# Kernel tuning notes

Measured on AMD Instinct MI355X. Metric: run time of the kernel, lower is better.

The kernel has to match this reference:

```python
import jax, jax.numpy as jnp
import numpy as np

DMIN, DMAX = -1.0, 1.0
B, I, O, K = 1024, 256, 256, 128

def setup_inputs() -> dict:
    key = jax.random.key(0)
    k1, k2, k3 = jax.random.split(key, 3)
    x = jax.random.normal(k1, (B, I), dtype=jnp.float32)
    bound = 1.0 / np.sqrt(I)
    base_weight = jax.random.uniform(k2, (O, I), dtype=jnp.float32, minval=-bound, maxval=bound)
    coeff = 0.03 * jax.random.normal(k3, (O, I, K), dtype=jnp.float32)
    coeff = coeff - coeff.mean(axis=-1, keepdims=True)
    return {
        'x': x,
        'base_weight': base_weight,
        'spline_coefficients': coeff,
        'spline_scale': jnp.ones((O, I), dtype=jnp.float32),
        'bias': jnp.zeros((O,), dtype=jnp.float32),
    }


def reference(x, base_weight, spline_coefficients, spline_scale, bias):
    num_knots = spline_coefficients.shape[-1]
    step = (DMAX - DMIN) / (num_knots - 1)
    # input activation (tanh) then clamp to spline domain
    p = jnp.tanh(x)                                   # (B, I)
    c = jnp.clip(p, DMIN, DMAX)
    scaled = (c - DMIN) / step                        # in [0, K-1]
    left = jnp.clip(jnp.floor(scaled).astype(jnp.int32), 0, num_knots - 1)
    right = jnp.minimum(left + 1, num_knots - 1)
    frac = scaled - left.astype(p.dtype)              # (B, I)
    # fold spline_scale into coefficients, then gather only the 2 relevant knots
    Cs = spline_coefficients * spline_scale[..., None]  # (O, I, K)
    ii = jnp.arange(x.shape[1])[None, :]                # (1, I) broadcasts with (B, I)
    cl = Cs[:, ii, left]                                # (O, B, I)
    cr = Cs[:, ii, right]                               # (O, B, I)
    spline = jnp.einsum('bi,obi->bo', 1.0 - frac, cl) + jnp.einsum('bi,obi->bo', frac, cr)
    base = jax.nn.silu(p) @ base_weight.T               # (B, O)
    return base + spline + bias[None, :]
```

## Files before the change

kernel.cpp:

```cpp
#include <hip/hip_runtime.h>

constexpr int Bb = 1024;
constexpr int Ii = 256;
constexpr int Oo = 256;
constexpr int Kk = 128;
constexpr int NCH = 8;

typedef unsigned short u16;
typedef unsigned int u32;
typedef u16 ushort4v __attribute__((ext_vector_type(4)));

__device__ __forceinline__ float bf16u_to_f(u16 u) {
    union { u32 ui; float f; } c;
    c.ui = ((u32)u) << 16;
    return c.f;
}
__device__ __forceinline__ u16 f_to_bf16(float f) {
    union { float f; u32 u; } c; c.f = f;
    u32 r = c.u + 0x7fffu + ((c.u >> 16) & 1u);
    return (u16)(r >> 16);
}

__global__ __launch_bounds__(256) void kperm(const float* __restrict__ cs,
                                             const float* __restrict__ scale,
                                             const float* __restrict__ wbase,
                                             u16* __restrict__ cp,
                                             float* __restrict__ wt) {
    __shared__ u16 T[128 * 66];
    int blk = blockIdx.x;
    int chunk = blk & 7;
    int sub = blk >> 3;
    int i  = chunk * 32 + (sub & 31);
    int oh = (sub >> 5) & 1, kh = (sub >> 6) & 1;
    int o0 = oh << 7, kb = kh << 6;
    int t = threadIdx.x;

    {
        int c4 = t & 15;
        int rb = t >> 4;
        const float4* cs4 = (const float4*)cs;
#pragma unroll
        for (int p = 0; p < 8; ++p) {
            int r = p * 16 + rb;
            int o = o0 + r;
            float sc = scale[o * Ii + i];
            float4 val = cs4[(size_t)(o * Ii + i) * (Kk / 4) + kh * 16 + c4];
            int kl = c4 * 4;
            T[r * 66 + kl + 0] = f_to_bf16(val.x * sc);
            T[r * 66 + kl + 1] = f_to_bf16(val.y * sc);
            T[r * 66 + kl + 2] = f_to_bf16(val.z * sc);
            T[r * 66 + kl + 3] = f_to_bf16(val.w * sc);
        }
    }
    __syncthreads();
    {
        int og = t & 63;
        int kg = t >> 6;
#pragma unroll
        for (int m = 0; m < 16; ++m) {
            int kl = kg * 16 + m;
            u32 lo = T[(og * 2) * 66 + kl];
            u32 hi = T[(og * 2 + 1) * 66 + kl];
            *(u32*)&cp[((size_t)i * Kk + kb + kl) * Oo + o0 + og * 2] = lo | (hi << 16);
        }
    }
    if (blk < 256) {
        int gid = blk * 256 + t;
        wt[gid] = wbase[(gid & 255) * Ii + (gid >> 8)];
    }
}

__global__ __launch_bounds__(256, 4) void kmain(const float* __restrict__ x,
                                                const char* __restrict__ cpb,
                                                const float* __restrict__ wt,
                                                float4* __restrict__ part4) {
    __shared__ float4 sf[256];
    __shared__ float wbuf[8 * 256];
    int t = threadIdx.x;
    int blk = blockIdx.x;
    int chunk = blk & (NCH - 1);
    int b0 = (blk >> 3) << 3;
    int i0 = chunk << 5;

    {
        int il = t & 31, bl = t >> 5;
        float xv = x[(size_t)(b0 + bl) * Ii + i0 + il];
        float e2 = __expf(2.f * xv);
        float p = 1.f - 2.f / (e2 + 1.f);
        float s = p / (1.f + __expf(-p));
        float c = fminf(fmaxf(p, -1.f), 1.f);
        float scaled = (c + 1.f) * ((float)(Kk - 1) * 0.5f);
        int l = (int)floorf(scaled);
        l = min(max(l, 0), Kk - 1);
        int rr = min(l + 1, Kk - 1);
        float4 v;
        v.x = scaled - (float)l;
        v.y = s;
        v.z = __int_as_float(l * (Oo * 2));
        v.w = __int_as_float(rr * (Oo * 2));
        sf[il * 8 + bl] = v;
    }

    int oq = t & 63;
    int bq = t >> 6;

    float a00=0.f,a01=0.f,a02=0.f,a03=0.f;
    float a10=0.f,a11=0.f,a12=0.f,a13=0.f;
    const char* cbase = cpb + (size_t)i0 * (Kk * Oo * 2) + oq * 8;

#pragma unroll
    for (int jb = 0; jb < 4; ++jb) {
        __syncthreads();
        {
            const float* wsrc = wt + (size_t)(i0 + jb * 8) * Oo;
#pragma unroll
            for (int p = 0; p < 8; ++p)
                wbuf[t + p * 256] = wsrc[t + p * 256];
        }
        __syncthreads();
#pragma unroll 4
        for (int m = 0; m < 8; ++m) {
            int il = jb * 8 + m;
            float4 v0 = sf[il * 8 + bq * 2];
            float4 v1 = sf[il * 8 + bq * 2 + 1];
            float4 w = *(const float4*)&wbuf[m * 256 + oq * 4];
            const char* ci = cbase + (size_t)il * (Kk * Oo * 2);
            ushort4v cl0 = *(const ushort4v*)(ci + __float_as_int(v0.z));
            ushort4v cr0 = *(const ushort4v*)(ci + __float_as_int(v0.w));
            ushort4v cl1 = *(const ushort4v*)(ci + __float_as_int(v1.z));
            ushort4v cr1 = *(const ushort4v*)(ci + __float_as_int(v1.w));
            float f0 = v0.x, g0 = 1.f - v0.x, s0 = v0.y;
            float f1 = v1.x, g1 = 1.f - v1.x, s1 = v1.y;
            a00 = fmaf(s0, w.x, a00); a01 = fmaf(s0, w.y, a01);
            a02 = fmaf(s0, w.z, a02); a03 = fmaf(s0, w.w, a03);
            a10 = fmaf(s1, w.x, a10); a11 = fmaf(s1, w.y, a11);
            a12 = fmaf(s1, w.z, a12); a13 = fmaf(s1, w.w, a13);
            a00 = fmaf(g0, bf16u_to_f(cl0.x), a00); a00 = fmaf(f0, bf16u_to_f(cr0.x), a00);
            a01 = fmaf(g0, bf16u_to_f(cl0.y), a01); a01 = fmaf(f0, bf16u_to_f(cr0.y), a01);
            a02 = fmaf(g0, bf16u_to_f(cl0.z), a02); a02 = fmaf(f0, bf16u_to_f(cr0.z), a02);
            a03 = fmaf(g0, bf16u_to_f(cl0.w), a03); a03 = fmaf(f0, bf16u_to_f(cr0.w), a03);
            a10 = fmaf(g1, bf16u_to_f(cl1.x), a10); a10 = fmaf(f1, bf16u_to_f(cr1.x), a10);
            a11 = fmaf(g1, bf16u_to_f(cl1.y), a11); a11 = fmaf(f1, bf16u_to_f(cr1.y), a11);
            a12 = fmaf(g1, bf16u_to_f(cl1.z), a12); a12 = fmaf(f1, bf16u_to_f(cr1.z), a12);
            a13 = fmaf(g1, bf16u_to_f(cl1.w), a13); a13 = fmaf(f1, bf16u_to_f(cr1.w), a13);
        }
    }
    size_t cstride = (size_t)(Bb * Oo / 4);
    float4 r0; r0.x=a00; r0.y=a01; r0.z=a02; r0.w=a03;
    float4 r1; r1.x=a10; r1.y=a11; r1.z=a12; r1.w=a13;
    part4[chunk * cstride + (size_t)(b0 + bq * 2) * (Oo / 4) + oq] = r0;
    part4[chunk * cstride + (size_t)(b0 + bq * 2 + 1) * (Oo / 4) + oq] = r1;
}

__global__ __launch_bounds__(256) void kreduce(const float4* __restrict__ part4,
                                               const float4* __restrict__ bias4,
                                               float4* __restrict__ out4) {
    int gid = blockIdx.x * 256 + threadIdx.x;
    const float4* p = part4 + gid;
    float4 s = p[0];
#pragma unroll
    for (int c = 1; c < NCH; ++c) {
        float4 v = p[(size_t)c * (Bb * Oo / 4)];
        s.x += v.x; s.y += v.y; s.z += v.z; s.w += v.w;
    }
    float4 bv = bias4[gid & 63];
    s.x += bv.x; s.y += bv.y; s.z += bv.z; s.w += bv.w;
    out4[gid] = s;
}

extern "C" void kernel_launch(void* const* d_in, const int* in_sizes, int n_in,
                              void* d_out, int out_size, void* d_ws, size_t ws_size,
                              hipStream_t stream) {
    const float* x     = (const float*)d_in[0];
    const float* wbase = (const float*)d_in[1];
    const float* coeff = (const float*)d_in[2];
    const float* scale = (const float*)d_in[3];
    const float* bias  = (const float*)d_in[4];
    float* out = (float*)d_out;

    char* ws = (char*)d_ws;
    u16*    cp    = (u16*)ws;
    float*  wt    = (float*)(ws + (16u << 20));
    float4* part4 = (float4*)(ws + (17u << 20));

    kperm<<<1024, 256, 0, stream>>>(coeff, scale, wbase, cp, wt);
    kmain<<<1024, 256, 0, stream>>>(x, (const char*)cp, wt, part4);
    kreduce<<<(Bb * Oo / 4) / 256, 256, 0, stream>>>(part4, (const float4*)bias, (float4*)out);
}
```

Baseline: 109.2 us.

## Fuse split-I reduction into main kernel via last-arrival atomic counter

Removes the separate reduce kernel launch. Each kmain block increments a per-batch-tile atomic counter after writing its partials, and the last of the eight chunk blocks for a tile sums the partials, adds the bias and writes the output. The counters are zeroed in kperm. This saves one kernel launch and its pass over global memory, at the cost of a threadfence, an atomic per block, and a serialized tail on the last-arriving block.

```diff
diff --git a/kernel.cpp b/kernel.cpp
--- a/kernel.cpp
+++ b/kernel.cpp
@@ -25,7 +25,8 @@
                                              const float* __restrict__ scale,
                                              const float* __restrict__ wbase,
                                              u16* __restrict__ cp,
-                                             float* __restrict__ wt) {
+                                             float* __restrict__ wt,
+                                             u32* __restrict__ cnt) {
     __shared__ u16 T[128 * 66];
     int blk = blockIdx.x;
     int chunk = blk & 7;
@@ -68,18 +69,24 @@
         int gid = blk * 256 + t;
         wt[gid] = wbase[(gid & 255) * Ii + (gid >> 8)];
     }
+    if (blk == 256 && t < 128) cnt[t] = 0;
 }
 
 __global__ __launch_bounds__(256, 4) void kmain(const float* __restrict__ x,
                                                 const char* __restrict__ cpb,
                                                 const float* __restrict__ wt,
-                                                float4* __restrict__ part4) {
+                                                float4* __restrict__ part4,
+                                                u32* __restrict__ cnt,
+                                                const float4* __restrict__ bias4,
+                                                float4* __restrict__ out4) {
     __shared__ float4 sf[256];
     __shared__ float wbuf[8 * 256];
+    __shared__ int lastArrival;
     int t = threadIdx.x;
     int blk = blockIdx.x;
     int chunk = blk & (NCH - 1);
-    int b0 = (blk >> 3) << 3;
+    int bt = blk >> 3;
+    int b0 = bt << 3;
     int i0 = chunk << 5;
 
     {
@@ -150,22 +157,33 @@
     float4 r1; r1.x=a10; r1.y=a11; r1.z=a12; r1.w=a13;
     part4[chunk * cstride + (size_t)(b0 + bq * 2) * (Oo / 4) + oq] = r0;
     part4[chunk * cstride + (size_t)(b0 + bq * 2 + 1) * (Oo / 4) + oq] = r1;
-}
-
-__global__ __launch_bounds__(256) void kreduce(const float4* __restrict__ part4,
-                                               const float4* __restrict__ bias4,
-                                               float4* __restrict__ out4) {
-    int gid = blockIdx.x * 256 + threadIdx.x;
-    const float4* p = part4 + gid;
-    float4 s = p[0];
-#pragma unroll
-    for (int c = 1; c < NCH; ++c) {
-        float4 v = p[(size_t)c * (Bb * Oo / 4)];
-        s.x += v.x; s.y += v.y; s.z += v.z; s.w += v.w;
-    }
-    float4 bv = bias4[gid & 63];
-    s.x += bv.x; s.y += bv.y; s.z += bv.z; s.w += bv.w;
-    out4[gid] = s;
+
+    __threadfence();
+    __syncthreads();
+    if (t == 0) {
+        u32 old = __hip_atomic_fetch_add(&cnt[bt], 1u, __ATOMIC_ACQ_REL,
+                                         __HIP_MEMORY_SCOPE_AGENT);
+        lastArrival = (old == (u32)(NCH - 1));
+    }
+    __syncthreads();
+    if (lastArrival) {
+        __threadfence();
+        const float4* p = part4 + (size_t)b0 * (Oo / 4);
+        float4* o4 = out4 + (size_t)b0 * (Oo / 4);
+#pragma unroll
+        for (int e = 0; e < 2; ++e) {
+            int idx = e * 256 + t;
+            float4 s = p[idx];
+#pragma unroll
+            for (int c = 1; c < NCH; ++c) {
+                float4 v = p[idx + (size_t)c * cstride];
+                s.x += v.x; s.y += v.y; s.z += v.z; s.w += v.w;
+            }
+            float4 bv = bias4[idx & 63];
+            s.x += bv.x; s.y += bv.y; s.z += bv.z; s.w += bv.w;
+            o4[idx] = s;
+        }
+    }
 }
 
 extern "C" void kernel_launch(void* const* d_in, const int* in_sizes, int n_in,
@@ -182,8 +200,9 @@
     u16*    cp    = (u16*)ws;
     float*  wt    = (float*)(ws + (16u << 20));
     float4* part4 = (float4*)(ws + (17u << 20));
-
-    kperm<<<1024, 256, 0, stream>>>(coeff, scale, wbase, cp, wt);
-    kmain<<<1024, 256, 0, stream>>>(x, (const char*)cp, wt, part4);
-    kreduce<<<(Bb * Oo / 4) / 256, 256, 0, stream>>>(part4, (const float4*)bias, (float4*)out);
-}
+    u32*    cnt   = (u32*)(ws + (25u << 20));
+
+    kperm<<<1024, 256, 0, stream>>>(coeff, scale, wbase, cp, wt, cnt);
+    kmain<<<1024, 256, 0, stream>>>(x, (const char*)cp, wt, part4, cnt,
+                                    (const float4*)bias, (float4*)out);
+}
```

Measured after the change: 261.7 us. +139.5%, slower.
